# Performance work log

Measured on AMD Instinct MI355X. Metric: run time of the kernel, lower is better.

Reference implementation:

```python
import jax, jax.numpy as jnp
import numpy as np

NUM_QUBITS = 7
LAYERS = 8
T = 32
BATCH = 32


def _entangling_matrix(n):
    """Product of CNOT-at-position layers: L0 @ L1 @ ... @ L_{n-2} (numpy, static)."""
    I2 = np.eye(2)
    CNOT = np.array([[1, 0, 0, 0], [0, 1, 0, 0], [0, 0, 0, 1], [0, 0, 1, 0]], dtype=np.float64)

    def layer(pos):
        mats = [I2] * n
        mats[pos] = CNOT
        del mats[pos + 1]
        out = np.eye(1)
        for m in mats:
            out = np.kron(out, m)
        return out

    E = np.eye(2 ** n)
    for i in reversed(range(n - 1)):
        E = layer(i) @ E
    return E


def _bkron(a, b):
    """Batched Kronecker product: a (..., p, q), b (..., r, s) -> (..., p*r, q*s)."""
    p, q = a.shape[-2], a.shape[-1]
    r, s = b.shape[-2], b.shape[-1]
    res = a[..., :, None, :, None] * b[..., None, :, None, :]
    return res.reshape(res.shape[:-4] + (p * r, q * s))


def _r3(angles):
    """angles (..., 3) = (omega, theta, phi) -> R3 matrices (..., 2, 2) complex64."""
    omega = angles[..., 0]
    theta = angles[..., 1]
    phi = angles[..., 2]
    e1 = jnp.exp(-1j * (phi + omega) / 2)  # == exp_factor_1; conj == exp_factor_4
    e2 = jnp.exp(1j * (phi - omega) / 2)   # == exp_factor_2; conj == exp_factor_3
    c = jnp.cos(theta / 2)
    s = jnp.sin(theta / 2)
    row1 = jnp.stack([e1 * c, -e2 * s], axis=-1)
    row2 = jnp.stack([jnp.conj(e2) * s, jnp.conj(e1) * c], axis=-1)
    return jnp.stack([row1, row2], axis=-2).astype(jnp.complex64)


def setup_inputs() -> dict:
    key = jax.random.key(0)
    k1, k2 = jax.random.split(key)
    params = jax.random.normal(k1, (T, BATCH, LAYERS, NUM_QUBITS, 3), dtype=jnp.float32)
    input_state = jax.random.normal(k2, (T * BATCH, 2 ** NUM_QUBITS), dtype=jnp.float32)
    return {"input_state": input_state, "params": params}


def reference(input_state, params):
    Tn, B, L, Q, _ = params.shape
    dim = 2 ** Q
    TB = Tn * B
    E = jnp.asarray(_entangling_matrix(Q), dtype=jnp.complex64)
    Einv = E.T  # E is real, so conj-transpose == transpose

    p = params.reshape(TB, L, Q, 3)
    r3 = _r3(p)  # (TB, L, Q, 2, 2) complex64

    matrix = jnp.broadcast_to(jnp.eye(dim, dtype=jnp.complex64), (TB, dim, dim))
    for l in range(L):
        # Rotation block: kron of per-qubit R3 gates -> (TB, dim, dim)
        rot = jnp.ones((TB, 1, 1), dtype=jnp.complex64)
        for q in range(Q):
            rot = _bkron(rot, r3[:, l, q])
        matrix = jnp.einsum('bij,bjk->bik', rot, matrix)
        Eop = E if l % 2 == 0 else Einv
        matrix = jnp.einsum('ij,bjk->bik', Eop, matrix)

    state = input_state.astype(jnp.complex64)  # (TB, dim)
    return jnp.einsum('bij,bj->bi', matrix, state)
```

## Files before the change

kernel.cpp:

```cpp
#include <hip/hip_runtime.h>

#define DIM    128
#define LAYERS 8
#define NQ     7

__device__ __forceinline__ int perm_g (int x) { x ^= x >> 1; x ^= x >> 2; x ^= x >> 4; return x; }
__device__ __forceinline__ int perm_gi(int x) { return x ^ (x >> 1); }

template<int M>
__device__ __forceinline__ float shfx(float x) {
    int v = __float_as_int(x); int r;
    if constexpr (M == 1)       r = __builtin_amdgcn_update_dpp(0, v, 0xB1, 0xF, 0xF, true);
    else if constexpr (M == 2)  r = __builtin_amdgcn_update_dpp(0, v, 0x4E, 0xF, 0xF, true);
    else if constexpr (M == 4)  r = __builtin_amdgcn_ds_swizzle(v, 0x101F);
    else if constexpr (M == 8)  r = __builtin_amdgcn_ds_swizzle(v, 0x201F);
    else if constexpr (M == 16) r = __builtin_amdgcn_ds_swizzle(v, 0x401F);
    else                        r = __shfl_xor(v, 32);
    return __int_as_float(r);
}

__device__ __forceinline__ float2 cmul2(float2 m0, float2 a, float2 m1, float2 b) {
    float2 r;
    r.x = m0.x * a.x - m0.y * a.y + m1.x * b.x - m1.y * b.y;
    r.y = m0.x * a.y + m0.y * a.x + m1.x * b.y + m1.y * b.x;
    return r;
}

template<int M>
__device__ __forceinline__ void butterfly(int L, float2& lo, float2& hi, float4 g) {
    const int bit = L & M;
    const float2 m0 = make_float2(g.x, g.y), m1 = make_float2(g.z, g.w);
    float2 plo, phl;
    plo.x = shfx<M>(lo.x); plo.y = shfx<M>(lo.y);
    phl.x = shfx<M>(hi.x); phl.y = shfx<M>(hi.y);
    const float2 a_lo = bit ? plo : lo,  b_lo = bit ? lo : plo;
    const float2 a_hi = bit ? phl : hi,  b_hi = bit ? hi : phl;
    lo = cmul2(m0, a_lo, m1, b_lo);
    hi = cmul2(m0, a_hi, m1, b_hi);
}

__global__ __launch_bounds__(64) void qsim_kernel(
        const float* __restrict__ state,
        const float* __restrict__ params,
        float* __restrict__ out,
        int TB) {
    __shared__ float4 gm[LAYERS * NQ][2];

    const int L  = threadIdx.x;
    const int bb = blockIdx.x;

    float2 lo = make_float2(state[bb * DIM + L],      0.0f);
    float2 hi = make_float2(state[bb * DIM + L + 64], 0.0f);

    if (L < LAYERS * NQ) {
        const float* pp = params + (size_t)bb * (LAYERS * NQ * 3) + L * 3;
        const float omega = pp[0], theta = pp[1], phi = pp[2];
        const float a = 0.5f * (phi + omega), b = 0.5f * (phi - omega), t = 0.5f * theta;
        const float sa = __sinf(a), ca = __cosf(a);
        const float sb = __sinf(b), cb = __cosf(b);
        const float st = __sinf(t), ct = __cosf(t);
        gm[L][0] = make_float4(ca * ct, -sa * ct, -cb * st, -sb * st);
        gm[L][1] = make_float4(cb * st, -sb * st,  ca * ct,  sa * ct);
    }
    __syncthreads();

    const int gL = perm_g (L),  gH = perm_g (L | 64) & 63;
    const int iL = perm_gi(L),  iH = perm_gi(L | 64) & 63;

    #pragma unroll
    for (int l = 0; l < LAYERS; ++l) {
        const int base = l * NQ;
        const float4 G0a = gm[base + 0][0];
        const float4 G0b = gm[base + 0][1];
        const float4 G1  = gm[base + 1][(L >> 5) & 1];
        const float4 G2  = gm[base + 2][(L >> 4) & 1];
        const float4 G3  = gm[base + 3][(L >> 3) & 1];
        const float4 G4  = gm[base + 4][(L >> 2) & 1];
        const float4 G5  = gm[base + 5][(L >> 1) & 1];
        const float4 G6  = gm[base + 6][L & 1];

        {
            const float2 nlo = cmul2(make_float2(G0a.x, G0a.y), lo, make_float2(G0a.z, G0a.w), hi);
            const float2 nhi = cmul2(make_float2(G0b.x, G0b.y), lo, make_float2(G0b.z, G0b.w), hi);
            lo = nlo; hi = nhi;
        }
        butterfly<32>(L, lo, hi, G1);
        butterfly<16>(L, lo, hi, G2);
        butterfly< 8>(L, lo, hi, G3);
        butterfly< 4>(L, lo, hi, G4);
        butterfly< 2>(L, lo, hi, G5);
        butterfly< 1>(L, lo, hi, G6);

        const int sl = (l & 1) ? iL : gL;
        const int sh = (l & 1) ? iH : gH;
        float2 nlo, nhi;
        nlo.x = __shfl(lo.x, sl); nlo.y = __shfl(lo.y, sl);
        nhi.x = __shfl(hi.x, sh); nhi.y = __shfl(hi.y, sh);
        lo = nlo; hi = nhi;
    }

    const size_t TOT = (size_t)TB * DIM;
    const size_t e   = (size_t)bb * DIM + L;
    out[e]            = lo.x;
    out[e + 64]       = hi.x;
    out[TOT + e]      = lo.y;
    out[TOT + e + 64] = hi.y;
}

extern "C" void kernel_launch(void* const* d_in, const int* in_sizes, int n_in,
                              void* d_out, int out_size, void* d_ws, size_t ws_size,
                              hipStream_t stream) {
    const float* input_state;
    const float* params;
    int TB;
    if (in_sizes[0] < in_sizes[1]) {
        input_state = (const float*)d_in[0];
        params      = (const float*)d_in[1];
        TB = in_sizes[0] / DIM;
    } else {
        params      = (const float*)d_in[0];
        input_state = (const float*)d_in[1];
        TB = in_sizes[1] / DIM;
    }
    float* out = (float*)d_out;

    qsim_kernel<<<TB, 64, 0, stream>>>(input_state, params, out, TB);
}
```

Measured before the change: 10.74 us.

## Eliminate per-layer entangling permutation shuffles by tracking permuted basis in butterflies

Removes the explicit per-layer bpermute (__shfl) that applied the CNOT-chain permutation. Instead the state is kept in a permuted basis on alternate layers, and the butterfly partners and gate row selection are rewritten as XOR masks (63, 31, 15, 7, 3, 1) that follow the Gray-code-like mapping. The exchanges use DPP row ops, ds_swizzle, and gfx950 v_permlane16/32_swap instructions instead of LDS-backed bpermute. This cuts cross-lane data movement per layer at the cost of more intricate index logic and inline asm that relies on specific hardware instructions.

```diff
diff --git a/kernel.cpp b/kernel.cpp
--- a/kernel.cpp
+++ b/kernel.cpp
@@ -4,39 +4,56 @@
 #define LAYERS 8
 #define NQ     7
 
-__device__ __forceinline__ int perm_g (int x) { x ^= x >> 1; x ^= x >> 2; x ^= x >> 4; return x; }
-__device__ __forceinline__ int perm_gi(int x) { return x ^ (x >> 1); }
+template<int CTRL>
+__device__ __forceinline__ float dpp_f(float x) {
+    return __int_as_float(__builtin_amdgcn_update_dpp(0, __float_as_int(x), CTRL, 0xF, 0xF, true));
+}
+__device__ __forceinline__ float swz31(float x) {
+    return __int_as_float(__builtin_amdgcn_ds_swizzle(__float_as_int(x), 0x7C1F));
+}
+__device__ __forceinline__ float permxor32(float x) {
+    float a = x, b = x;
+    asm("s_nop 1\n\tv_permlane32_swap_b32 %0, %1" : "+v"(a), "+v"(b));
+    return (a + b) - x;
+}
+__device__ __forceinline__ float permxor16(float x) {
+    float a = x, b = x;
+    asm("s_nop 1\n\tv_permlane16_swap_b32 %0, %1" : "+v"(a), "+v"(b));
+    return (a + b) - x;
+}
 
 template<int M>
 __device__ __forceinline__ float shfx(float x) {
-    int v = __float_as_int(x); int r;
-    if constexpr (M == 1)       r = __builtin_amdgcn_update_dpp(0, v, 0xB1, 0xF, 0xF, true);
-    else if constexpr (M == 2)  r = __builtin_amdgcn_update_dpp(0, v, 0x4E, 0xF, 0xF, true);
-    else if constexpr (M == 4)  r = __builtin_amdgcn_ds_swizzle(v, 0x101F);
-    else if constexpr (M == 8)  r = __builtin_amdgcn_ds_swizzle(v, 0x201F);
-    else if constexpr (M == 16) r = __builtin_amdgcn_ds_swizzle(v, 0x401F);
-    else                        r = __shfl_xor(v, 32);
-    return __int_as_float(r);
+    if constexpr      (M == 1)  return dpp_f<0xB1>(x);
+    else if constexpr (M == 2)  return dpp_f<0x4E>(x);
+    else if constexpr (M == 3)  return dpp_f<0x1B>(x);
+    else if constexpr (M == 4)  return dpp_f<0x141>(dpp_f<0x1B>(x));
+    else if constexpr (M == 7)  return dpp_f<0x141>(x);
+    else if constexpr (M == 8)  return dpp_f<0x128>(x);
+    else if constexpr (M == 15) return dpp_f<0x140>(x);
+    else if constexpr (M == 16) return permxor16(x);
+    else if constexpr (M == 31) return swz31(x);
+    else if constexpr (M == 32) return permxor32(x);
+    else                        return permxor32(swz31(x));
 }
 
-__device__ __forceinline__ float2 cmul2(float2 m0, float2 a, float2 m1, float2 b) {
+__device__ __forceinline__ float2 rowmul(float4 G, float2 c0, float2 c1) {
     float2 r;
-    r.x = m0.x * a.x - m0.y * a.y + m1.x * b.x - m1.y * b.y;
-    r.y = m0.x * a.y + m0.y * a.x + m1.x * b.y + m1.y * b.x;
+    r.x = G.x * c0.x - G.y * c0.y + G.z * c1.x - G.w * c1.y;
+    r.y = G.x * c0.y + G.y * c0.x + G.z * c1.y + G.w * c1.x;
     return r;
 }
-
+__device__ __forceinline__ float2 bfly(float2 v, float2 p, int rv, float4 G) {
+    return rv ? rowmul(G, p, v) : rowmul(G, v, p);
+}
 template<int M>
-__device__ __forceinline__ void butterfly(int L, float2& lo, float2& hi, float4 g) {
-    const int bit = L & M;
-    const float2 m0 = make_float2(g.x, g.y), m1 = make_float2(g.z, g.w);
+__device__ __forceinline__ void bstep(float2& lo, float2& hi, int rlo, int rhi,
+                                      float4 Glo, float4 Ghi) {
     float2 plo, phl;
     plo.x = shfx<M>(lo.x); plo.y = shfx<M>(lo.y);
     phl.x = shfx<M>(hi.x); phl.y = shfx<M>(hi.y);
-    const float2 a_lo = bit ? plo : lo,  b_lo = bit ? lo : plo;
-    const float2 a_hi = bit ? phl : hi,  b_hi = bit ? hi : phl;
-    lo = cmul2(m0, a_lo, m1, b_lo);
-    hi = cmul2(m0, a_hi, m1, b_hi);
+    lo = bfly(lo, plo, rlo, Glo);
+    hi = bfly(hi, phl, rhi, Ghi);
 }
 
 __global__ __launch_bounds__(64) void qsim_kernel(
@@ -64,39 +81,56 @@
     }
     __syncthreads();
 
-    const int gL = perm_g (L),  gH = perm_g (L | 64) & 63;
-    const int iL = perm_gi(L),  iH = perm_gi(L | 64) & 63;
-
     #pragma unroll
     for (int l = 0; l < LAYERS; ++l) {
         const int base = l * NQ;
-        const float4 G0a = gm[base + 0][0];
-        const float4 G0b = gm[base + 0][1];
-        const float4 G1  = gm[base + 1][(L >> 5) & 1];
-        const float4 G2  = gm[base + 2][(L >> 4) & 1];
-        const float4 G3  = gm[base + 3][(L >> 3) & 1];
-        const float4 G4  = gm[base + 4][(L >> 2) & 1];
-        const float4 G5  = gm[base + 5][(L >> 1) & 1];
-        const float4 G6  = gm[base + 6][L & 1];
-
-        {
-            const float2 nlo = cmul2(make_float2(G0a.x, G0a.y), lo, make_float2(G0a.z, G0a.w), hi);
-            const float2 nhi = cmul2(make_float2(G0b.x, G0b.y), lo, make_float2(G0b.z, G0b.w), hi);
+        const float4 R0 = gm[base][0];
+        const float4 R1 = gm[base][1];
+        if ((l & 1) == 0) {
+            const int b5 = (L >> 5) & 1, b4 = (L >> 4) & 1, b3 = (L >> 3) & 1;
+            const int b2 = (L >> 2) & 1, b1 = (L >> 1) & 1, b0 = L & 1;
+            const float4 G1 = gm[base + 1][b5];
+            const float4 G2 = gm[base + 2][b4];
+            const float4 G3 = gm[base + 3][b3];
+            const float4 G4 = gm[base + 4][b2];
+            const float4 G5 = gm[base + 5][b1];
+            const float4 G6 = gm[base + 6][b0];
+            const float2 nlo = rowmul(R0, lo, hi);
+            const float2 nhi = rowmul(R1, lo, hi);
             lo = nlo; hi = nhi;
+            bstep<32>(lo, hi, b5, b5, G1, G1);
+            bstep<16>(lo, hi, b4, b4, G2, G2);
+            bstep< 8>(lo, hi, b3, b3, G3, G3);
+            bstep< 4>(lo, hi, b2, b2, G4, G4);
+            bstep< 2>(lo, hi, b1, b1, G5, G5);
+            bstep< 1>(lo, hi, b0, b0, G6, G6);
+        } else {
+            const int r5 = (L >> 5) & 1;
+            const int r4 = ((L >> 4) ^ (L >> 5)) & 1;
+            const int r3 = ((L >> 3) ^ (L >> 4)) & 1;
+            const int r2 = ((L >> 2) ^ (L >> 3)) & 1;
+            const int r1 = ((L >> 1) ^ (L >> 2)) & 1;
+            const int r0 = (L ^ (L >> 1)) & 1;
+            const float4 G1a = gm[base + 1][r5];
+            const float4 G1b = gm[base + 1][r5 ^ 1];
+            const float4 G2  = gm[base + 2][r4];
+            const float4 G3  = gm[base + 3][r3];
+            const float4 G4  = gm[base + 4][r2];
+            const float4 G5  = gm[base + 5][r1];
+            const float4 G6  = gm[base + 6][r0];
+            float2 lo63, hi63;
+            lo63.x = shfx<63>(lo.x); lo63.y = shfx<63>(lo.y);
+            hi63.x = shfx<63>(hi.x); hi63.y = shfx<63>(hi.y);
+            const float2 nlo = rowmul(R0, lo, hi63);
+            const float2 nhi = rowmul(R1, lo63, hi);
+            lo = nlo; hi = nhi;
+            bstep<63>(lo, hi, r5, r5 ^ 1, G1a, G1b);
+            bstep<31>(lo, hi, r4, r4, G2, G2);
+            bstep<15>(lo, hi, r3, r3, G3, G3);
+            bstep< 7>(lo, hi, r2, r2, G4, G4);
+            bstep< 3>(lo, hi, r1, r1, G5, G5);
+            bstep< 1>(lo, hi, r0, r0, G6, G6);
         }
-        butterfly<32>(L, lo, hi, G1);
-        butterfly<16>(L, lo, hi, G2);
-        butterfly< 8>(L, lo, hi, G3);
-        butterfly< 4>(L, lo, hi, G4);
-        butterfly< 2>(L, lo, hi, G5);
-        butterfly< 1>(L, lo, hi, G6);
-
-        const int sl = (l & 1) ? iL : gL;
-        const int sh = (l & 1) ? iH : gH;
-        float2 nlo, nhi;
-        nlo.x = __shfl(lo.x, sl); nlo.y = __shfl(lo.y, sl);
-        nhi.x = __shfl(hi.x, sh); nhi.y = __shfl(hi.y, sh);
-        lo = nlo; hi = nhi;
     }
 
     const size_t TOT = (size_t)TB * DIM;
```

After: 10.87 us. Within noise of the previous version (+1.2%).
